# Performance work log

Measured on AMD Instinct MI355X. Metric: run time of the kernel, lower is better.

## Reference

```python
import jax, jax.numpy as jnp
import numpy as np

N_NODES = 10000
N_EDGES = 640000
IN_DIM = 128
HID = 128
N_GRAPHS = 64


def setup_inputs() -> dict:
    key = jax.random.key(0)
    ks = jax.random.split(key, 9)
    x = jax.random.normal(ks[0], (N_NODES, IN_DIM), dtype=jnp.float32)
    edge_index = jax.random.randint(ks[1], (2, N_EDGES), 0, N_NODES, dtype=jnp.int32)
    batch = jnp.sort(jax.random.randint(ks[2], (N_NODES,), 0, N_GRAPHS, dtype=jnp.int32))
    # GCNConv weights (glorot-ish init) and zero biases
    W0 = jax.random.normal(ks[3], (IN_DIM, HID), dtype=jnp.float32) / np.float32(np.sqrt(IN_DIM))
    b0 = jnp.zeros((HID,), dtype=jnp.float32)
    W1 = jax.random.normal(ks[4], (HID, HID), dtype=jnp.float32) / np.float32(np.sqrt(HID))
    b1 = jnp.zeros((HID,), dtype=jnp.float32)
    W2 = jax.random.normal(ks[5], (HID, HID), dtype=jnp.float32) / np.float32(np.sqrt(HID))
    b2 = jnp.zeros((HID,), dtype=jnp.float32)
    return {"x": x, "edge_index": edge_index, "batch": batch,
            "W0": W0, "b0": b0, "W1": W1, "b1": b1, "W2": W2, "b2": b2}


def _gcn_conv(x, src, dst, W, b, n_nodes):
    """PyG GCNConv: self-loops + symmetric normalization, then linear+bias."""
    h = x @ W  # [N, H]
    # degree of destination nodes, +1 for the added self-loop
    deg = jax.ops.segment_sum(jnp.ones((src.shape[0],), h.dtype), dst,
                              num_segments=n_nodes) + 1.0
    dis = jax.lax.rsqrt(deg)  # deg >= 1 so no inf guard needed
    # messages along real edges, normalized by dis[src]*dis[dst]
    msg = h[src] * (dis[src] * dis[dst])[:, None]  # [E, H]
    out = jax.ops.segment_sum(msg, dst, num_segments=n_nodes)
    # self-loop contribution: dis[i]^2 * h[i]
    out = out + h * (dis * dis)[:, None]
    return out + b


def reference(x, edge_index, batch, W0, b0, W1, b1, W2, b2):
    src, dst = edge_index[0], edge_index[1]
    n_nodes = x.shape[0]
    # layer 0 and 1 followed by ReLU (dropout: eval mode -> identity)
    h = _gcn_conv(x, src, dst, W0, b0, n_nodes)
    h = jax.nn.relu(h)
    h = _gcn_conv(h, src, dst, W1, b1, n_nodes)
    h = jax.nn.relu(h)
    h = _gcn_conv(h, src, dst, W2, b2, n_nodes)
    # global mean pool over batch indices
    sums = jax.ops.segment_sum(h, batch, num_segments=N_GRAPHS)  # [B, H]
    counts = jax.ops.segment_sum(jnp.ones((n_nodes,), h.dtype), batch,
                                 num_segments=N_GRAPHS)
    return sums / jnp.maximum(counts, 1.0)[:, None]
```

## Files before the change

kernel.cpp:

```cpp
#include <hip/hip_runtime.h>
#include <hip/hip_fp16.h>

#define NN 10000
#define NE 640000
#define NG 64
#define CAP 128
#define NB 625
#define BCAP 1280

typedef _Float16 f16x8 __attribute__((ext_vector_type(8)));
typedef float f32x4 __attribute__((ext_vector_type(4)));

__device__ __forceinline__ void split8v(float4 xa, float4 xb, f16x8& ah, f16x8& al) {
    float x[8] = {xa.x, xa.y, xa.z, xa.w, xb.x, xb.y, xb.z, xb.w};
#pragma unroll
    for (int j = 0; j < 8; j++) {
        ah[j] = (_Float16)x[j];
        al[j] = (_Float16)(x[j] - (float)ah[j]);
    }
}

__global__ __launch_bounds__(256) void k_initp1(
    const int* __restrict__ batch, int* __restrict__ gstart,
    const float* __restrict__ W0, const float* __restrict__ W1, const float* __restrict__ W2,
    __half* __restrict__ wh, __half* __restrict__ wl,
    const int* __restrict__ ei, int* __restrict__ bcur, int* __restrict__ pk,
    __half* __restrict__ g16a, __half* __restrict__ g16b)
{
    __shared__ int hist[NB];
    int bid = blockIdx.x, t = threadIdx.x;
    if (bid < 40) {
        int i = bid * 256 + t;
        if (i < NN) {
            int b = batch[i];
            int prev = (i == 0) ? -1 : batch[i - 1];
            for (int g = prev + 1; g <= b; g++) gstart[g] = i;
            if (i == NN - 1)
                for (int g = b + 1; g <= NG; g++) gstart[g] = NN;
        }
    } else if (bid < 232) {
        int wid = bid - 40;
        int z = wid >> 6;
        int q = (wid & 63) * 256 + t;
        int c = q >> 7, k = q & 127;
        const float* W = (z == 0) ? W0 : (z == 1) ? W1 : W2;
        float v = W[k * 128 + c];
        __half h = __float2half(v);
        __half lo = __float2half(v - __half2float(h));
        wh[z * 16384 + c * 128 + k] = h;
        wl[z * 16384 + c * 128 + k] = lo;
    } else if (bid < 389) {
        for (int q = t; q < NB; q += 256) hist[q] = 0;
        __syncthreads();
        int4 s4[4], d4[4];
        int ebase = (bid - 232) * 4096;
#pragma unroll
        for (int q = 0; q < 4; q++) {
            int e = ebase + q * 1024 + t * 4;
            if (e < NE) {
                s4[q] = *(const int4*)&ei[e];
                d4[q] = *(const int4*)&ei[NE + e];
                atomicAdd(&hist[d4[q].x >> 4], 1);
                atomicAdd(&hist[d4[q].y >> 4], 1);
                atomicAdd(&hist[d4[q].z >> 4], 1);
                atomicAdd(&hist[d4[q].w >> 4], 1);
            }
        }
        __syncthreads();
        for (int q = t; q < NB; q += 256) {
            int h = hist[q];
            hist[q] = (h > 0) ? atomicAdd(&bcur[q], h) : 0;
        }
        __syncthreads();
#pragma unroll
        for (int q = 0; q < 4; q++) {
            int e = ebase + q * 1024 + t * 4;
            if (e < NE) {
                int b0i = d4[q].x >> 4, b1i = d4[q].y >> 4, b2i = d4[q].z >> 4, b3i = d4[q].w >> 4;
                int r0 = atomicAdd(&hist[b0i], 1);
                int r1 = atomicAdd(&hist[b1i], 1);
                int r2 = atomicAdd(&hist[b2i], 1);
                int r3 = atomicAdd(&hist[b3i], 1);
                if (r0 < BCAP) pk[b0i * BCAP + r0] = s4[q].x | ((d4[q].x & 15) << 14);
                if (r1 < BCAP) pk[b1i * BCAP + r1] = s4[q].y | ((d4[q].y & 15) << 14);
                if (r2 < BCAP) pk[b2i * BCAP + r2] = s4[q].z | ((d4[q].z & 15) << 14);
                if (r3 < BCAP) pk[b3i * BCAP + r3] = s4[q].w | ((d4[q].w & 15) << 14);
            }
        }
    } else {
        uint4 z = {0u, 0u, 0u, 0u};
        ((uint4*)(g16a + NN * 128))[t] = z;
        ((uint4*)(g16b + NN * 128))[t] = z;
    }
}

__global__ __launch_bounds__(512) void k_p2g0(
    const int* __restrict__ bcur, const int* __restrict__ pk,
    const float* __restrict__ x,
    const __half* __restrict__ whT, const __half* __restrict__ wlT,
    const float* __restrict__ b2, const int* __restrict__ gstart,
    int* __restrict__ deg, int* __restrict__ csrc, __half* __restrict__ g16a,
    float* __restrict__ out)
{
    __shared__ int buf[16 * CAP];
    __shared__ int cnt[16];
    int b = blockIdx.x, t = threadIdx.x;
    if (b == 0) {
        for (int q = t; q < NG * 128; q += 512) {
            int g = q >> 7;
            out[q] = (gstart[g + 1] > gstart[g]) ? b2[q & 127] : 0.f;
        }
    }
    if (t < 16) cnt[t] = 0;
    __syncthreads();

    int n = bcur[b];
    if (n > BCAP) n = BCAP;
    const int* pb = &pk[b * BCAP];
    for (int i = t; i < n; i += 512) {
        int v = pb[i];
        int nd = v >> 14;
        int slot = atomicAdd(&cnt[nd], 1);
        if (slot < CAP) buf[(nd << 7) + slot] = v & 0x3FFF;
    }
    __syncthreads();

    int node0 = b << 4;
    if (t < 16) {
        int c = cnt[t];
        deg[node0 + t] = c;
        buf[(t << 7) + min(c, CAP - 1)] = NN;
    }
    __syncthreads();

    ((int4*)&csrc[node0 << 7])[t] = ((const int4*)buf)[t];

    int w = t >> 6, l = t & 63, lr = l & 15, lg = l >> 4;
    int cw = w * 16;
    const _Float16* whp = (const _Float16*)whT;
    const _Float16* wlp = (const _Float16*)wlT;
    f32x4 acc = {0.f, 0.f, 0.f, 0.f};
#pragma unroll
    for (int ks = 0; ks < 4; ks++) {
        int kb = ks * 32 + lg * 8;
        f16x8 ah, al;
        split8v(*(const float4*)&x[(node0 + lr) * 128 + kb],
                *(const float4*)&x[(node0 + lr) * 128 + kb + 4], ah, al);
        int c0 = cw + lr;
        f16x8 bh = *(const f16x8*)&whp[c0 * 128 + kb];
        f16x8 bl = *(const f16x8*)&wlp[c0 * 128 + kb];
        acc = __builtin_amdgcn_mfma_f32_16x16x32_f16(ah, bh, acc, 0, 0, 0);
        acc = __builtin_amdgcn_mfma_f32_16x16x32_f16(al, bh, acc, 0, 0, 0);
        acc = __builtin_amdgcn_mfma_f32_16x16x32_f16(ah, bl, acc, 0, 0, 0);
    }
#pragma unroll
    for (int reg = 0; reg < 4; reg++) {
        int row = lg * 4 + reg;
        float d = rsqrtf((float)cnt[row] + 1.0f);
        g16a[(node0 + row) * 128 + cw + lr] = __float2half(acc[reg] * d);
    }
}

__device__ __forceinline__ void accp(uint2 v, float2& p, float2& q) {
    float2 f0 = __half22float2(*(__half2*)&v.x);
    float2 f1 = __half22float2(*(__half2*)&v.y);
    p.x += f0.x; p.y += f0.y; q.x += f1.x; q.y += f1.y;
}

__global__ __launch_bounds__(512) void k_ag(
    const __half* __restrict__ gin, const float* __restrict__ bias,
    const int* __restrict__ deg, const int* __restrict__ csrc,
    const __half* __restrict__ whT, const __half* __restrict__ wlT,
    __half* __restrict__ gout)
{
    __shared__ float Xs[16][132];
    int base = blockIdx.x << 4;
    int t = threadIdx.x;
    int w = t >> 6, l = t & 63;
    int half = l >> 5, li = l & 31;
    int co = li * 4;
#pragma unroll
    for (int k4 = 0; k4 < 2; k4++) {
        int row = w * 2 + k4;
        int i = base + row;
        int dgi = __builtin_amdgcn_readfirstlane(deg[i]);
        int nn_ = min(dgi, CAP - 1);
        int np = (nn_ + 1) & ~1;
        float2 A0 = {0.f, 0.f}, A1 = {0.f, 0.f};
        float2 B0 = {0.f, 0.f}, B1 = {0.f, 0.f};
        if (half == 0) {
            uint2 sv = *(const uint2*)&gin[i * 128 + co];
            A0 = __half22float2(*(__half2*)&sv.x);
            A1 = __half22float2(*(__half2*)&sv.y);
        }
        const int* cp = &csrc[i << 7];
        for (int bs = 0; bs < np; bs += 64) {
            int m = np - bs;
            if (m > 64) m = 64;
            int myedge = (l < m) ? cp[bs + l] : NN;
            int pairs = m >> 1;
            int j = 0;
            for (; j + 8 <= pairs; j += 8) {
                int r0 = __shfl(myedge, 2 * j + half);
                int r1 = __shfl(myedge, 2 * j + 2 + half);
                int r2 = __shfl(myedge, 2 * j + 4 + half);
                int r3 = __shfl(myedge, 2 * j + 6 + half);
                int r4 = __shfl(myedge, 2 * j + 8 + half);
                int r5 = __shfl(myedge, 2 * j + 10 + half);
                int r6 = __shfl(myedge, 2 * j + 12 + half);
                int r7 = __shfl(myedge, 2 * j + 14 + half);
                uint2 v0 = *(const uint2*)&gin[r0 * 128 + co];
                uint2 v1 = *(const uint2*)&gin[r1 * 128 + co];
                uint2 v2 = *(const uint2*)&gin[r2 * 128 + co];
                uint2 v3 = *(const uint2*)&gin[r3 * 128 + co];
                uint2 v4 = *(const uint2*)&gin[r4 * 128 + co];
                uint2 v5 = *(const uint2*)&gin[r5 * 128 + co];
                uint2 v6 = *(const uint2*)&gin[r6 * 128 + co];
                uint2 v7 = *(const uint2*)&gin[r7 * 128 + co];
                accp(v0, A0, A1); accp(v1, B0, B1);
                accp(v2, A0, A1); accp(v3, B0, B1);
                accp(v4, A0, A1); accp(v5, B0, B1);
                accp(v6, A0, A1); accp(v7, B0, B1);
            }
            for (; j < pairs; j++) {
                int r = __shfl(myedge, 2 * j + half);
                uint2 v = *(const uint2*)&gin[r * 128 + co];
                accp(v, A0, A1);
            }
        }
        A0.x += B0.x; A0.y += B0.y; A1.x += B1.x; A1.y += B1.y;
        A0.x += __shfl_xor(A0.x, 32);
        A0.y += __shfl_xor(A0.y, 32);
        A1.x += __shfl_xor(A1.x, 32);
        A1.y += __shfl_xor(A1.y, 32);
        if (half == 0) {
            float di = rsqrtf((float)dgi + 1.0f);
            float4 bb = *(const float4*)&bias[co];
            float4 o;
            o.x = fmaxf(di * A0.x + bb.x, 0.f);
            o.y = fmaxf(di * A0.y + bb.y, 0.f);
            o.z = fmaxf(di * A1.x + bb.z, 0.f);
            o.w = fmaxf(di * A1.y + bb.w, 0.f);
            *(float4*)&Xs[row][co] = o;
        }
    }
    __syncthreads();

    int lr = l & 15, lg = l >> 4;
    int cw = w * 16;
    const _Float16* whp = (const _Float16*)whT;
    const _Float16* wlp = (const _Float16*)wlT;
    f32x4 acc = {0.f, 0.f, 0.f, 0.f};
#pragma unroll
    for (int ks = 0; ks < 4; ks++) {
        int kb = ks * 32 + lg * 8;
        f16x8 ah, al;
        split8v(*(const float4*)&Xs[lr][kb], *(const float4*)&Xs[lr][kb + 4], ah, al);
        int c0 = cw + lr;
        f16x8 bh = *(const f16x8*)&whp[c0 * 128 + kb];
        f16x8 bl = *(const f16x8*)&wlp[c0 * 128 + kb];
        acc = __builtin_amdgcn_mfma_f32_16x16x32_f16(ah, bh, acc, 0, 0, 0);
        acc = __builtin_amdgcn_mfma_f32_16x16x32_f16(al, bh, acc, 0, 0, 0);
        acc = __builtin_amdgcn_mfma_f32_16x16x32_f16(ah, bl, acc, 0, 0, 0);
    }
#pragma unroll
    for (int reg = 0; reg < 4; reg++) {
        int row = lg * 4 + reg;
        float d = rsqrtf((float)deg[base + row] + 1.0f);
        gout[(base + row) * 128 + cw + lr] = __float2half(acc[reg] * d);
    }
}

__global__ __launch_bounds__(512) void k_aggpool(const __half* __restrict__ g16,
                                                 const int* __restrict__ deg,
                                                 const int* __restrict__ csrc,
                                                 const int* __restrict__ batch,
                                                 const int* __restrict__ gstart,
                                                 float* __restrict__ out) {
    __shared__ float sm[16][128];
    __shared__ int gid[16];
    int base = blockIdx.x << 4;
    int t = threadIdx.x;
    int w = t >> 6, l = t & 63;
    int half = l >> 5, li = l & 31;
    int co = li * 4;
#pragma unroll
    for (int k4 = 0; k4 < 2; k4++) {
        int row = w * 2 + k4;
        int i = base + row;
        int dgi = __builtin_amdgcn_readfirstlane(deg[i]);
        int n = min(dgi, CAP - 1);
        int np = (n + 1) & ~1;
        float2 A0 = {0.f, 0.f}, A1 = {0.f, 0.f};
        float2 B0 = {0.f, 0.f}, B1 = {0.f, 0.f};
        if (half == 0) {
            uint2 sv = *(const uint2*)&g16[i * 128 + co];
            A0 = __half22float2(*(__half2*)&sv.x);
            A1 = __half22float2(*(__half2*)&sv.y);
        }
        const int* cp = &csrc[i << 7];
        for (int bs = 0; bs < np; bs += 64) {
            int m = np - bs;
            if (m > 64) m = 64;
            int myedge = (l < m) ? cp[bs + l] : NN;
            int pairs = m >> 1;
            int j = 0;
            for (; j + 8 <= pairs; j += 8) {
                int r0 = __shfl(myedge, 2 * j + half);
                int r1 = __shfl(myedge, 2 * j + 2 + half);
                int r2 = __shfl(myedge, 2 * j + 4 + half);
                int r3 = __shfl(myedge, 2 * j + 6 + half);
                int r4 = __shfl(myedge, 2 * j + 8 + half);
                int r5 = __shfl(myedge, 2 * j + 10 + half);
                int r6 = __shfl(myedge, 2 * j + 12 + half);
                int r7 = __shfl(myedge, 2 * j + 14 + half);
                uint2 v0 = *(const uint2*)&g16[r0 * 128 + co];
                uint2 v1 = *(const uint2*)&g16[r1 * 128 + co];
                uint2 v2 = *(const uint2*)&g16[r2 * 128 + co];
                uint2 v3 = *(const uint2*)&g16[r3 * 128 + co];
                uint2 v4 = *(const uint2*)&g16[r4 * 128 + co];
                uint2 v5 = *(const uint2*)&g16[r5 * 128 + co];
                uint2 v6 = *(const uint2*)&g16[r6 * 128 + co];
                uint2 v7 = *(const uint2*)&g16[r7 * 128 + co];
                accp(v0, A0, A1); accp(v1, B0, B1);
                accp(v2, A0, A1); accp(v3, B0, B1);
                accp(v4, A0, A1); accp(v5, B0, B1);
                accp(v6, A0, A1); accp(v7, B0, B1);
            }
            for (; j < pairs; j++) {
                int r = __shfl(myedge, 2 * j + half);
                uint2 v = *(const uint2*)&g16[r * 128 + co];
                accp(v, A0, A1);
            }
        }
        A0.x += B0.x; A0.y += B0.y; A1.x += B1.x; A1.y += B1.y;
        A0.x += __shfl_xor(A0.x, 32);
        A0.y += __shfl_xor(A0.y, 32);
        A1.x += __shfl_xor(A1.x, 32);
        A1.y += __shfl_xor(A1.y, 32);
        if (half == 0) {
            float di = rsqrtf((float)dgi + 1.0f);
            int g = batch[i];
            float icnt = 1.0f / (float)max(gstart[g + 1] - gstart[g], 1);
            float s = di * icnt;
            float4 o;
            o.x = s * A0.x;
            o.y = s * A0.y;
            o.z = s * A1.x;
            o.w = s * A1.y;
            *(float4*)&sm[row][co] = o;
            if (li == 0) gid[row] = g;
        }
    }
    __syncthreads();

    if (t < 128) {
        float acc = sm[0][t];
        int g = gid[0];
#pragma unroll
        for (int r = 1; r < 16; r++) {
            if (gid[r] == g) {
                acc += sm[r][t];
            } else {
                atomicAdd(&out[(g << 7) + t], acc);
                g = gid[r];
                acc = sm[r][t];
            }
        }
        atomicAdd(&out[(g << 7) + t], acc);
    }
}

extern "C" void kernel_launch(void* const* d_in, const int* in_sizes, int n_in,
                              void* d_out, int out_size, void* d_ws, size_t ws_size,
                              hipStream_t stream) {
    const float* x     = (const float*)d_in[0];
    const int*   ei    = (const int*)d_in[1];
    const int*   batch = (const int*)d_in[2];
    const float* W0 = (const float*)d_in[3];
    const float* b0 = (const float*)d_in[4];
    const float* W1 = (const float*)d_in[5];
    const float* b1 = (const float*)d_in[6];
    const float* W2 = (const float*)d_in[7];
    const float* b2 = (const float*)d_in[8];
    float* out = (float*)d_out;

    float* ws    = (float*)d_ws;
    int*   deg   = (int*)ws;
    int*   gstart= (int*)(ws + 10240);
    int*   bcur  = (int*)(ws + 10320);
    int*   csrc  = (int*)(ws + 10960);
    __half* g16a = (__half*)(ws + 1290960);
    __half* g16b = (__half*)(ws + 1931984);
    int*   pk    = (int*)(ws + 2573008);
    __half* wh   = (__half*)(ws + 3373008);
    __half* wlo  = (__half*)(ws + 3397584);

    hipMemsetAsync(bcur, 0, 640 * sizeof(int), stream);
    k_initp1<<<390, 256, 0, stream>>>(batch, gstart, W0, W1, W2, wh, wlo, ei, bcur, pk,
                                      g16a, g16b);
    k_p2g0<<<NB, 512, 0, stream>>>(bcur, pk, x, wh, wlo, b2, gstart, deg, csrc, g16a, out);
    k_ag<<<NB, 512, 0, stream>>>(g16a, b0, deg, csrc, wh + 16384, wlo + 16384, g16b);
    k_ag<<<NB, 512, 0, stream>>>(g16b, b1, deg, csrc, wh + 32768, wlo + 32768, g16a);
    k_aggpool<<<NB, 512, 0, stream>>>(g16a, deg, csrc, batch, gstart, out);
}
```

Before: 167.0 us.

## Replace global-atomic bucket binning with fixed per-block slots, drop memset

Edge binning no longer reserves space with global atomics on a bucket cursor. Each binning block now writes into its own fixed 32-entry slot inside every destination bucket and records a per-block count. The consumer kernel scans all 157 slots per bucket and skips empty entries. This removes the memset, one sync pass and the global atomics, at the cost of a larger sparse pk array that the consumer must read, plus silent truncation if a block puts more than 32 edges into one bucket.

```diff
diff --git a/kernel.cpp b/kernel.cpp
--- a/kernel.cpp
+++ b/kernel.cpp
@@ -6,7 +6,8 @@
 #define NG 64
 #define CAP 128
 #define NB 625
-#define BCAP 1280
+#define PKB 32
+#define NPB 157
 
 typedef _Float16 f16x8 __attribute__((ext_vector_type(8)));
 typedef float f32x4 __attribute__((ext_vector_type(4)));
@@ -24,10 +25,10 @@
     const int* __restrict__ batch, int* __restrict__ gstart,
     const float* __restrict__ W0, const float* __restrict__ W1, const float* __restrict__ W2,
     __half* __restrict__ wh, __half* __restrict__ wl,
-    const int* __restrict__ ei, int* __restrict__ bcur, int* __restrict__ pk,
+    const int* __restrict__ ei, int* __restrict__ pk, int* __restrict__ cntbb,
     __half* __restrict__ g16a, __half* __restrict__ g16b)
 {
-    __shared__ int hist[NB];
+    __shared__ int cur[NB];
     int bid = blockIdx.x, t = threadIdx.x;
     if (bid < 40) {
         int i = bid * 256 + t;
@@ -50,43 +51,29 @@
         wh[z * 16384 + c * 128 + k] = h;
         wl[z * 16384 + c * 128 + k] = lo;
     } else if (bid < 389) {
-        for (int q = t; q < NB; q += 256) hist[q] = 0;
+        int blk = bid - 232;
+        for (int q = t; q < NB; q += 256) cur[q] = 0;
         __syncthreads();
-        int4 s4[4], d4[4];
-        int ebase = (bid - 232) * 4096;
+        int ebase = blk * 4096;
 #pragma unroll
         for (int q = 0; q < 4; q++) {
             int e = ebase + q * 1024 + t * 4;
             if (e < NE) {
-                s4[q] = *(const int4*)&ei[e];
-                d4[q] = *(const int4*)&ei[NE + e];
-                atomicAdd(&hist[d4[q].x >> 4], 1);
-                atomicAdd(&hist[d4[q].y >> 4], 1);
-                atomicAdd(&hist[d4[q].z >> 4], 1);
-                atomicAdd(&hist[d4[q].w >> 4], 1);
+                int4 s4 = *(const int4*)&ei[e];
+                int4 d4 = *(const int4*)&ei[NE + e];
+                int b0 = d4.x >> 4, b1 = d4.y >> 4, b2 = d4.z >> 4, b3 = d4.w >> 4;
+                int r0 = atomicAdd(&cur[b0], 1);
+                int r1 = atomicAdd(&cur[b1], 1);
+                int r2 = atomicAdd(&cur[b2], 1);
+                int r3 = atomicAdd(&cur[b3], 1);
+                if (r0 < PKB) pk[b0 * (NPB * PKB) + blk * PKB + r0] = s4.x | ((d4.x & 15) << 14);
+                if (r1 < PKB) pk[b1 * (NPB * PKB) + blk * PKB + r1] = s4.y | ((d4.y & 15) << 14);
+                if (r2 < PKB) pk[b2 * (NPB * PKB) + blk * PKB + r2] = s4.z | ((d4.z & 15) << 14);
+                if (r3 < PKB) pk[b3 * (NPB * PKB) + blk * PKB + r3] = s4.w | ((d4.w & 15) << 14);
             }
         }
         __syncthreads();
-        for (int q = t; q < NB; q += 256) {
-            int h = hist[q];
-            hist[q] = (h > 0) ? atomicAdd(&bcur[q], h) : 0;
-        }
-        __syncthreads();
-#pragma unroll
-        for (int q = 0; q < 4; q++) {
-            int e = ebase + q * 1024 + t * 4;
-            if (e < NE) {
-                int b0i = d4[q].x >> 4, b1i = d4[q].y >> 4, b2i = d4[q].z >> 4, b3i = d4[q].w >> 4;
-                int r0 = atomicAdd(&hist[b0i], 1);
-                int r1 = atomicAdd(&hist[b1i], 1);
-                int r2 = atomicAdd(&hist[b2i], 1);
-                int r3 = atomicAdd(&hist[b3i], 1);
-                if (r0 < BCAP) pk[b0i * BCAP + r0] = s4[q].x | ((d4[q].x & 15) << 14);
-                if (r1 < BCAP) pk[b1i * BCAP + r1] = s4[q].y | ((d4[q].y & 15) << 14);
-                if (r2 < BCAP) pk[b2i * BCAP + r2] = s4[q].z | ((d4[q].z & 15) << 14);
-                if (r3 < BCAP) pk[b3i * BCAP + r3] = s4[q].w | ((d4[q].w & 15) << 14);
-            }
-        }
+        for (int q = t; q < NB; q += 256) cntbb[q * NPB + blk] = min(cur[q], PKB);
     } else {
         uint4 z = {0u, 0u, 0u, 0u};
         ((uint4*)(g16a + NN * 128))[t] = z;
@@ -95,7 +82,7 @@
 }
 
 __global__ __launch_bounds__(512) void k_p2g0(
-    const int* __restrict__ bcur, const int* __restrict__ pk,
+    const int* __restrict__ cntbb, const int* __restrict__ pk,
     const float* __restrict__ x,
     const __half* __restrict__ whT, const __half* __restrict__ wlT,
     const float* __restrict__ b2, const int* __restrict__ gstart,
@@ -104,6 +91,7 @@
 {
     __shared__ int buf[16 * CAP];
     __shared__ int cnt[16];
+    __shared__ unsigned char cw[NPB + 3];
     int b = blockIdx.x, t = threadIdx.x;
     if (b == 0) {
         for (int q = t; q < NG * 128; q += 512) {
@@ -112,16 +100,18 @@
         }
     }
     if (t < 16) cnt[t] = 0;
-    __syncthreads();
-
-    int n = bcur[b];
-    if (n > BCAP) n = BCAP;
-    const int* pb = &pk[b * BCAP];
-    for (int i = t; i < n; i += 512) {
-        int v = pb[i];
-        int nd = v >> 14;
-        int slot = atomicAdd(&cnt[nd], 1);
-        if (slot < CAP) buf[(nd << 7) + slot] = v & 0x3FFF;
+    if (t < NPB) cw[t] = (unsigned char)cntbb[b * NPB + t];
+    __syncthreads();
+
+    const int* pb = &pk[b * (NPB * PKB)];
+    for (int idx = t; idx < NPB * PKB; idx += 512) {
+        int blk = idx >> 5, s = idx & 31;
+        if (s < (int)cw[blk]) {
+            int v = pb[idx];
+            int nd = v >> 14;
+            int slot = atomicAdd(&cnt[nd], 1);
+            if (slot < CAP) buf[(nd << 7) + slot] = v & 0x3FFF;
+        }
     }
     __syncthreads();
 
@@ -136,7 +126,7 @@
     ((int4*)&csrc[node0 << 7])[t] = ((const int4*)buf)[t];
 
     int w = t >> 6, l = t & 63, lr = l & 15, lg = l >> 4;
-    int cw = w * 16;
+    int cw2 = w * 16;
     const _Float16* whp = (const _Float16*)whT;
     const _Float16* wlp = (const _Float16*)wlT;
     f32x4 acc = {0.f, 0.f, 0.f, 0.f};
@@ -146,7 +136,7 @@
         f16x8 ah, al;
         split8v(*(const float4*)&x[(node0 + lr) * 128 + kb],
                 *(const float4*)&x[(node0 + lr) * 128 + kb + 4], ah, al);
-        int c0 = cw + lr;
+        int c0 = cw2 + lr;
         f16x8 bh = *(const f16x8*)&whp[c0 * 128 + kb];
         f16x8 bl = *(const f16x8*)&wlp[c0 * 128 + kb];
         acc = __builtin_amdgcn_mfma_f32_16x16x32_f16(ah, bh, acc, 0, 0, 0);
@@ -157,7 +147,7 @@
     for (int reg = 0; reg < 4; reg++) {
         int row = lg * 4 + reg;
         float d = rsqrtf((float)cnt[row] + 1.0f);
-        g16a[(node0 + row) * 128 + cw + lr] = __float2half(acc[reg] * d);
+        g16a[(node0 + row) * 128 + cw2 + lr] = __float2half(acc[reg] * d);
     }
 }
 
@@ -388,18 +378,17 @@
     float* ws    = (float*)d_ws;
     int*   deg   = (int*)ws;
     int*   gstart= (int*)(ws + 10240);
-    int*   bcur  = (int*)(ws + 10320);
     int*   csrc  = (int*)(ws + 10960);
     __half* g16a = (__half*)(ws + 1290960);
     __half* g16b = (__half*)(ws + 1931984);
     int*   pk    = (int*)(ws + 2573008);
-    __half* wh   = (__half*)(ws + 3373008);
-    __half* wlo  = (__half*)(ws + 3397584);
-
-    hipMemsetAsync(bcur, 0, 640 * sizeof(int), stream);
-    k_initp1<<<390, 256, 0, stream>>>(batch, gstart, W0, W1, W2, wh, wlo, ei, bcur, pk,
+    int*   cntbb = (int*)(ws + 5713008);
+    __half* wh   = (__half*)(ws + 5811136);
+    __half* wlo  = (__half*)(ws + 5835712);
+
+    k_initp1<<<390, 256, 0, stream>>>(batch, gstart, W0, W1, W2, wh, wlo, ei, pk, cntbb,
                                       g16a, g16b);
-    k_p2g0<<<NB, 512, 0, stream>>>(bcur, pk, x, wh, wlo, b2, gstart, deg, csrc, g16a, out);
+    k_p2g0<<<NB, 512, 0, stream>>>(cntbb, pk, x, wh, wlo, b2, gstart, deg, csrc, g16a, out);
     k_ag<<<NB, 512, 0, stream>>>(g16a, b0, deg, csrc, wh + 16384, wlo + 16384, g16b);
     k_ag<<<NB, 512, 0, stream>>>(g16b, b1, deg, csrc, wh + 32768, wlo + 32768, g16a);
     k_aggpool<<<NB, 512, 0, stream>>>(g16a, deg, csrc, batch, gstart, out);
```

New measurement: 168.5 us. Within noise of the previous version (+0.9%).
